# Performance work log

Hardware: AMD Instinct MI355X
Metric: run time of the kernel (lower is better)

Reference implementation:

```python
import jax, jax.numpy as jnp
import numpy as np

EPS = 1e-6


def setup_inputs() -> dict:
    key = jax.random.key(0)
    k1, k2, k3 = jax.random.split(key, 3)
    B, N1, N2, D, K, C = 8, 1024, 1024, 1, 5, 3
    xa = jax.random.normal(k1, (B, N1, D, C), dtype=jnp.float32)
    features = jax.random.normal(k2, (B, N1, K, C), dtype=jnp.float32)
    xt = jax.random.normal(k3, (B, N2, D, C), dtype=jnp.float32)
    # learned parameter: log_std of shape (in_dims, num_basis, num_channels)
    log_std = jnp.log(1e-6 + 0.1 * jnp.ones((D, K, C), dtype=jnp.float32))
    return {"xa": xa, "features": features, "xt": xt, "log_std": log_std}


def reference(xa, features, xt, log_std):
    # xa: (B, N1, D, C), xt: (B, N2, D, C), features: (B, N1, K, C), log_std: (D, K, C)
    std = jnp.exp(log_std) + EPS                       # (D, K, C)
    x1 = xa[:, :, :, None, :] / std                    # (B, N1, D, K, C)
    x2 = xt[:, :, :, None, :] / std                    # (B, N2, D, K, C)
    sq1 = jnp.sum(x1 * x1, axis=2)                     # (B, N1, K, C)
    sq2 = jnp.sum(x2 * x2, axis=2)                     # (B, N2, K, C)
    # pairwise squared distance per basis/channel
    prod = jnp.einsum('bndkc,bmdkc->bnmkc', x1, x2)    # (B, N1, N2, K, C)
    dist = sq1[:, :, None] + sq2[:, None] - 2.0 * prod # (B, N1, N2, K, C)
    wt = jnp.exp(-0.5 * dist)                          # RBF weights
    # weighted sum over context points N1
    smoothed = jnp.einsum('bnkc,bnmkc->bmkc', features, wt)  # (B, N2, K, C)
    return smoothed
```

## Files before the change

### kernel.cpp

```cpp
#include <hip/hip_runtime.h>

#define EPS_F 1e-6f
#define LOG2E 1.4426950408889634f

typedef float f4a __attribute__((ext_vector_type(4), aligned(16)));

__device__ __forceinline__ float rfl(float x) {
    return __builtin_bit_cast(float, __builtin_amdgcn_readfirstlane(__builtin_bit_cast(int, x)));
}

__global__ __launch_bounds__(256, 4) void icgp_partial_kernel(
    const float* __restrict__ xa,
    const float* __restrict__ feat,
    const float* __restrict__ xt,
    const float* __restrict__ log_std,
    float* __restrict__ pws)
{
    __shared__ float lds[3840];

    const int bid  = blockIdx.x;
    const int nsb  = bid & 7;
    const int mt   = (bid >> 3) & 15;
    const int b    = bid >> 7;
    const int tid  = threadIdx.x;
    const int wv   = tid >> 6;
    const int lane = tid & 63;
    const int m    = mt * 64 + lane;
    const int n0   = nsb * 128;

    const float* __restrict__ fg = feat + ((size_t)b * 1024 + n0) * 15;
    for (int j = tid; j < 480; j += 256) {
        const f4a v = *(const f4a*)(fg + j * 4);
        #pragma unroll
        for (int e = 0; e < 4; ++e) {
            const int g = j * 4 + e;
            const int r = g / 15, c = g - r * 15;
            lds[r * 16 + c] = v[e];
        }
    }
    const float* __restrict__ ag = xa + ((size_t)b * 1024 + n0) * 3;
    if (tid < 96) {
        const f4a v = *(const f4a*)(ag + tid * 4);
        #pragma unroll
        for (int e = 0; e < 4; ++e) {
            const int g = tid * 4 + e;
            const int r = g / 3, c = g - r * 3;
            lds[2048 + r * 4 + c] = v[e];
        }
    }

    float coef[15];
    #pragma unroll
    for (int kc = 0; kc < 15; ++kc) {
        const float s = __expf(log_std[kc]) + EPS_F;
        coef[kc] = rfl(-0.5f * LOG2E / (s * s));
    }
    bool uni = true;
    #pragma unroll
    for (int k = 1; k < 5; ++k)
        #pragma unroll
        for (int c = 0; c < 3; ++c)
            uni = uni && (coef[k * 3 + c] == coef[c]);

    const float t0 = xt[(b * 1024 + m) * 3 + 0];
    const float t1 = xt[(b * 1024 + m) * 3 + 1];
    const float t2 = xt[(b * 1024 + m) * 3 + 2];

    __syncthreads();

    float acc[15];
    #pragma unroll
    for (int kc = 0; kc < 15; ++kc) acc[kc] = 0.0f;

    const int rb = wv * 32;

    if (uni) {
        const float c0 = coef[0], c1 = coef[1], c2 = coef[2];
        #pragma unroll 8
        for (int i = 0; i < 32; ++i) {
            const float* __restrict__ row = &lds[(rb + i) * 16];
            const f4a fA = *(const f4a*)(row);
            const f4a fB = *(const f4a*)(row + 4);
            const f4a fC = *(const f4a*)(row + 8);
            const f4a fD = *(const f4a*)(row + 12);
            const f4a av = *(const f4a*)(&lds[2048 + (rb + i) * 4]);
            float d0 = av.x - t0; d0 *= d0;
            float d1 = av.y - t1; d1 *= d1;
            float d2 = av.z - t2; d2 *= d2;
            const float w0 = __builtin_amdgcn_exp2f(d0 * c0);
            const float w1 = __builtin_amdgcn_exp2f(d1 * c1);
            const float w2 = __builtin_amdgcn_exp2f(d2 * c2);
            acc[0]  += w0 * fA.x;  acc[1]  += w1 * fA.y;  acc[2]  += w2 * fA.z;
            acc[3]  += w0 * fA.w;  acc[4]  += w1 * fB.x;  acc[5]  += w2 * fB.y;
            acc[6]  += w0 * fB.z;  acc[7]  += w1 * fB.w;  acc[8]  += w2 * fC.x;
            acc[9]  += w0 * fC.y;  acc[10] += w1 * fC.z;  acc[11] += w2 * fC.w;
            acc[12] += w0 * fD.x;  acc[13] += w1 * fD.y;  acc[14] += w2 * fD.z;
        }
    } else {
        for (int i = 0; i < 32; ++i) {
            const float* __restrict__ row = &lds[(rb + i) * 16];
            float fv[16];
            *(f4a*)(fv)      = *(const f4a*)(row);
            *(f4a*)(fv + 4)  = *(const f4a*)(row + 4);
            *(f4a*)(fv + 8)  = *(const f4a*)(row + 8);
            *(f4a*)(fv + 12) = *(const f4a*)(row + 12);
            const f4a av = *(const f4a*)(&lds[2048 + (rb + i) * 4]);
            float dd[3];
            dd[0] = av.x - t0; dd[0] *= dd[0];
            dd[1] = av.y - t1; dd[1] *= dd[1];
            dd[2] = av.z - t2; dd[2] *= dd[2];
            #pragma unroll
            for (int k = 0; k < 5; ++k)
                #pragma unroll
                for (int c = 0; c < 3; ++c)
                    acc[k * 3 + c] +=
                        __builtin_amdgcn_exp2f(dd[c] * coef[k * 3 + c]) * fv[k * 3 + c];
        }
    }

    __syncthreads();
    #pragma unroll
    for (int kc = 0; kc < 15; ++kc) lds[tid * 15 + kc] = acc[kc];
    __syncthreads();

    float* __restrict__ pb = pws + (size_t)nsb * 122880
                                 + ((size_t)b * 1024 + mt * 64) * 15;
    #pragma unroll
    for (int j = 0; j < 4; ++j) {
        const int oidx = j * 256 + tid;
        if (oidx < 960) {
            const int mm = oidx / 15, kc = oidx - mm * 15;
            float s = 0.0f;
            #pragma unroll
            for (int w = 0; w < 4; ++w)
                s += lds[(w * 64 + mm) * 15 + kc];
            pb[oidx] = s;
        }
    }
}

__global__ __launch_bounds__(256) void icgp_reduce_kernel(
    const float* __restrict__ pws, float* __restrict__ out)
{
    const int idx = blockIdx.x * 256 + threadIdx.x;
    float s = 0.0f;
    #pragma unroll
    for (int ns = 0; ns < 8; ++ns)
        s += pws[(size_t)ns * 122880 + idx];
    out[idx] = s;
}

extern "C" void kernel_launch(void* const* d_in, const int* in_sizes, int n_in,
                              void* d_out, int out_size, void* d_ws, size_t ws_size,
                              hipStream_t stream) {
    const float* xa      = (const float*)d_in[0];
    const float* feat    = (const float*)d_in[1];
    const float* xt      = (const float*)d_in[2];
    const float* log_std = (const float*)d_in[3];
    float* out = (float*)d_out;
    float* pws = (float*)d_ws;

    icgp_partial_kernel<<<dim3(1024), dim3(256), 0, stream>>>(xa, feat, xt, log_std, pws);
    icgp_reduce_kernel<<<dim3(480), dim3(256), 0, stream>>>(pws, out);
}
```

Before: 73.22 us.

## Fuse partial and reduce kernels into one block per batch-target tile

After: 76.51 us. +4.5%, slower.

```diff
diff --git a/kernel.cpp b/kernel.cpp
--- a/kernel.cpp
+++ b/kernel.cpp
@@ -9,27 +9,25 @@
     return __builtin_bit_cast(float, __builtin_amdgcn_readfirstlane(__builtin_bit_cast(int, x)));
 }
 
-__global__ __launch_bounds__(256, 4) void icgp_partial_kernel(
+__global__ __launch_bounds__(1024, 4) void icgp_fused_kernel(
     const float* __restrict__ xa,
     const float* __restrict__ feat,
     const float* __restrict__ xt,
     const float* __restrict__ log_std,
-    float* __restrict__ pws)
+    float* __restrict__ out)
 {
-    __shared__ float lds[3840];
+    __shared__ float lds[20480];
 
     const int bid  = blockIdx.x;
-    const int nsb  = bid & 7;
-    const int mt   = (bid >> 3) & 15;
-    const int b    = bid >> 7;
+    const int mt   = bid & 15;
+    const int b    = bid >> 4;
     const int tid  = threadIdx.x;
-    const int wv   = tid >> 6;
+    const int wv   = __builtin_amdgcn_readfirstlane(tid >> 6);
     const int lane = tid & 63;
     const int m    = mt * 64 + lane;
-    const int n0   = nsb * 128;
 
-    const float* __restrict__ fg = feat + ((size_t)b * 1024 + n0) * 15;
-    for (int j = tid; j < 480; j += 256) {
+    const float* __restrict__ fg = feat + (size_t)b * 15360;
+    for (int j = tid; j < 3840; j += 1024) {
         const f4a v = *(const f4a*)(fg + j * 4);
         #pragma unroll
         for (int e = 0; e < 4; ++e) {
@@ -38,14 +36,14 @@
             lds[r * 16 + c] = v[e];
         }
     }
-    const float* __restrict__ ag = xa + ((size_t)b * 1024 + n0) * 3;
-    if (tid < 96) {
+    const float* __restrict__ ag = xa + (size_t)b * 3072;
+    if (tid < 768) {
         const f4a v = *(const f4a*)(ag + tid * 4);
         #pragma unroll
         for (int e = 0; e < 4; ++e) {
             const int g = tid * 4 + e;
             const int r = g / 3, c = g - r * 3;
-            lds[2048 + r * 4 + c] = v[e];
+            lds[16384 + r * 4 + c] = v[e];
         }
     }
 
@@ -72,18 +70,18 @@
     #pragma unroll
     for (int kc = 0; kc < 15; ++kc) acc[kc] = 0.0f;
 
-    const int rb = wv * 32;
+    const int rb = wv * 64;
 
     if (uni) {
         const float c0 = coef[0], c1 = coef[1], c2 = coef[2];
-        #pragma unroll 8
-        for (int i = 0; i < 32; ++i) {
+        #pragma unroll 4
+        for (int i = 0; i < 64; ++i) {
             const float* __restrict__ row = &lds[(rb + i) * 16];
             const f4a fA = *(const f4a*)(row);
             const f4a fB = *(const f4a*)(row + 4);
             const f4a fC = *(const f4a*)(row + 8);
             const f4a fD = *(const f4a*)(row + 12);
-            const f4a av = *(const f4a*)(&lds[2048 + (rb + i) * 4]);
+            const f4a av = *(const f4a*)(&lds[16384 + (rb + i) * 4]);
             float d0 = av.x - t0; d0 *= d0;
             float d1 = av.y - t1; d1 *= d1;
             float d2 = av.z - t2; d2 *= d2;
@@ -97,14 +95,14 @@
             acc[12] += w0 * fD.x;  acc[13] += w1 * fD.y;  acc[14] += w2 * fD.z;
         }
     } else {
-        for (int i = 0; i < 32; ++i) {
+        for (int i = 0; i < 64; ++i) {
             const float* __restrict__ row = &lds[(rb + i) * 16];
             float fv[16];
             *(f4a*)(fv)      = *(const f4a*)(row);
             *(f4a*)(fv + 4)  = *(const f4a*)(row + 4);
             *(f4a*)(fv + 8)  = *(const f4a*)(row + 8);
             *(f4a*)(fv + 12) = *(const f4a*)(row + 12);
-            const f4a av = *(const f4a*)(&lds[2048 + (rb + i) * 4]);
+            const f4a av = *(const f4a*)(&lds[16384 + (rb + i) * 4]);
             float dd[3];
             dd[0] = av.x - t0; dd[0] *= dd[0];
             dd[1] = av.y - t1; dd[1] *= dd[1];
@@ -120,34 +118,17 @@
 
     __syncthreads();
     #pragma unroll
-    for (int kc = 0; kc < 15; ++kc) lds[tid * 15 + kc] = acc[kc];
+    for (int kc = 0; kc < 15; ++kc)
+        lds[wv * 960 + lane * 15 + kc] = acc[kc];
     __syncthreads();
 
-    float* __restrict__ pb = pws + (size_t)nsb * 122880
-                                 + ((size_t)b * 1024 + mt * 64) * 15;
-    #pragma unroll
-    for (int j = 0; j < 4; ++j) {
-        const int oidx = j * 256 + tid;
-        if (oidx < 960) {
-            const int mm = oidx / 15, kc = oidx - mm * 15;
-            float s = 0.0f;
-            #pragma unroll
-            for (int w = 0; w < 4; ++w)
-                s += lds[(w * 64 + mm) * 15 + kc];
-            pb[oidx] = s;
-        }
+    if (tid < 960) {
+        float s = 0.0f;
+        #pragma unroll
+        for (int w = 0; w < 16; ++w)
+            s += lds[w * 960 + tid];
+        out[(size_t)b * 15360 + mt * 960 + tid] = s;
     }
-}
-
-__global__ __launch_bounds__(256) void icgp_reduce_kernel(
-    const float* __restrict__ pws, float* __restrict__ out)
-{
-    const int idx = blockIdx.x * 256 + threadIdx.x;
-    float s = 0.0f;
-    #pragma unroll
-    for (int ns = 0; ns < 8; ++ns)
-        s += pws[(size_t)ns * 122880 + idx];
-    out[idx] = s;
 }
 
 extern "C" void kernel_launch(void* const* d_in, const int* in_sizes, int n_in,
@@ -158,8 +139,7 @@
     const float* xt      = (const float*)d_in[2];
     const float* log_std = (const float*)d_in[3];
     float* out = (float*)d_out;
-    float* pws = (float*)d_ws;
+    (void)d_ws; (void)ws_size;
 
-    icgp_partial_kernel<<<dim3(1024), dim3(256), 0, stream>>>(xa, feat, xt, log_std, pws);
-    icgp_reduce_kernel<<<dim3(480), dim3(256), 0, stream>>>(pws, out);
+    icgp_fused_kernel<<<dim3(128), dim3(1024), 0, stream>>>(xa, feat, xt, log_std, out);
 }
```
